# Kernel tuning notes

Measured on AMD Instinct MI355X. Metric: run time of the kernel, lower is better.

The kernel has to match this reference:

```python
import jax, jax.numpy as jnp
import numpy as np

D_THRE = 0.1       # compatibility distance threshold
RATIO = 1.0        # fraction of points kept as seeds
NUM_ITERS = 10     # power-iteration steps
NMS_RADIUS = 0.1   # NMS suppression radius
N_PTS = 6144


def _pairwise_dist(p):
    # p: [N, d] -> [N, N] euclidean distance matrix
    diff = p[:, None, :] - p[None, :, :]
    return jnp.linalg.norm(diff, axis=-1)


def setup_inputs() -> dict:
    key = jax.random.key(0)
    k1, k2 = jax.random.split(key)
    ipts2d = jax.random.uniform(k1, (N_PTS, 2), dtype=jnp.float32)
    ipts3d = jax.random.uniform(k2, (N_PTS, 3), dtype=jnp.float32)
    return {"ipts2d": ipts2d, "ipts3d": ipts3d}


def reference(ipts2d, ipts3d):
    N = ipts2d.shape[0]
    p2d_dist = _pairwise_dist(ipts2d)[None]            # [1, N, N]
    p3d_dist = _pairwise_dist(ipts3d)[None]            # [1, N, N]
    cross_dist = jnp.abs(p2d_dist - p3d_dist)          # [1, N, N]
    SC_measure = jnp.clip(1.0 - cross_dist ** 2 / D_THRE ** 2, 0.0, None)
    hard_SC = (cross_dist < D_THRE).astype(jnp.float32)

    # leading eigenvector via power iteration (fixed iteration count;
    # the torch allclose early-exit is a perf shortcut, same math)
    v0 = jnp.ones((1, N, 1), dtype=SC_measure.dtype)

    def body(i, v):
        v = jnp.matmul(SC_measure, v)                  # [1, N, 1]
        return v / (jnp.linalg.norm(v, axis=1, keepdims=True) + 1e-6)

    v = jax.lax.fori_loop(0, NUM_ITERS, body, v0)
    confidence = v[..., 0]                             # [1, N]

    # NMS seed picking (bs = 1)
    scores = confidence
    score_relation = (scores.T >= scores) | (p2d_dist[0] >= NMS_RADIUS)
    is_local_max = jnp.min(score_relation, axis=-1).astype(jnp.float32)
    score_local_max = scores * is_local_max            # [1, N]
    max_num = int(N * RATIO)
    seeds = jnp.argsort(-score_local_max, axis=1)[:, :max_num]  # [1, max_num]

    # seed gather + dense GEMM (computed as in the original; output unused)
    hard_SC_tight = (cross_dist < D_THRE / 2).astype(jnp.float32)
    seed_hard = hard_SC[:, seeds[0], :]                # [1, max_num, N]
    seed_hard_tight = hard_SC_tight[:, seeds[0], :]    # [1, max_num, N]
    SC2_measure = jnp.matmul(seed_hard_tight, hard_SC_tight) * seed_hard
    del SC2_measure  # original discards it and returns confidence

    return confidence
```

## Files before the change

### kernel.cpp

```cpp
#include <hip/hip_runtime.h>

#define NPTS 6144
#define RESCALE (1.0f / 1024.0f)

#define NIB 24
#define NJB 24
#define BI  256
#define BJ  256
#define MI  4
#define JT  (BJ / 16)
#define ROWU 20
#define LDS_U32 (2 * BJ * ROWU + BJ)

typedef unsigned short u16;
typedef unsigned int   u32;
typedef float v2f    __attribute__((ext_vector_type(2)));
typedef short bf16x8 __attribute__((ext_vector_type(8)));
typedef float f32x4  __attribute__((ext_vector_type(4)));

__device__ __forceinline__ u16 bsplit(float& x) {
  u32 u = __float_as_uint(x) & 0xFFFF0000u;
  x -= __uint_as_float(u);
  return (u16)(u >> 16);
}
__device__ __forceinline__ u32 pk(u16 lo, u16 hi) { return (u32)lo | ((u32)hi << 16); }

__device__ __forceinline__ void build_i(float x2, float y2, float x3, float y3,
                                        float z3, u32* __restrict__ a2,
                                        u32* __restrict__ a3) {
  float n2 = fmaf(x2, x2, y2 * y2);
  float n3 = fmaf(x3, x3, fmaf(y3, y3, z3 * z3));
  const u16 ONE = 0x3F80;
  float t;
  t = -2.f * x2; u16 AXH = bsplit(t), AXM = bsplit(t), AXL = bsplit(t);
  t = -2.f * y2; u16 AYH = bsplit(t), AYM = bsplit(t), AYL = bsplit(t);
  t = n2;        u16 N2H = bsplit(t), N2M = bsplit(t), N2L = bsplit(t);
  t = -2.f * x3; u16 CXH = bsplit(t), CXM = bsplit(t), CXL = bsplit(t);
  t = -2.f * y3; u16 CYH = bsplit(t), CYM = bsplit(t), CYL = bsplit(t);
  t = -2.f * z3; u16 CZH = bsplit(t), CZM = bsplit(t), CZL = bsplit(t);
  t = n3;        u16 N3H = bsplit(t), N3M = bsplit(t), N3L = bsplit(t);
  a2[0] = pk(AXH, AYH); a2[1] = pk(AXM, AYM); a2[2] = pk(AXH, AYH); a2[3] = pk(AXM, AYM);
  a2[4] = pk(AXL, AYL); a2[5] = pk(AXH, AYH); a2[6] = pk(N2H, N2M); a2[7] = pk(N2L, ONE);
  a2[8] = pk(ONE, ONE);
#pragma unroll
  for (int q = 9; q < 16; ++q) a2[q] = 0u;
  a3[0] = pk(CXH, CYH); a3[1]  = pk(CZH, CXM); a3[2]  = pk(CYM, CZM); a3[3]  = pk(CXH, CYH);
  a3[4] = pk(CZH, CXM); a3[5]  = pk(CYM, CZM); a3[6]  = pk(CXL, CYL); a3[7]  = pk(CZL, CXH);
  a3[8] = pk(CYH, CZH); a3[9]  = pk(N3H, N3M); a3[10] = pk(N3L, ONE); a3[11] = pk(ONE, ONE);
#pragma unroll
  for (int q = 12; q < 16; ++q) a3[q] = 0u;
}

__device__ __forceinline__ void build_j(float x2, float y2, float x3, float y3,
                                        float z3, u32* __restrict__ b2,
                                        u32* __restrict__ b3) {
  float n2 = fmaf(x2, x2, y2 * y2);
  float n3 = fmaf(x3, x3, fmaf(y3, y3, z3 * z3));
  const u16 ONE = 0x3F80;
  float t;
  t = x2; u16 BXH = bsplit(t), BXM = bsplit(t), BXL = bsplit(t);
  t = y2; u16 BYH = bsplit(t), BYM = bsplit(t), BYL = bsplit(t);
  t = n2; u16 N2H = bsplit(t), N2M = bsplit(t), N2L = bsplit(t);
  t = x3; u16 DXH = bsplit(t), DXM = bsplit(t), DXL = bsplit(t);
  t = y3; u16 DYH = bsplit(t), DYM = bsplit(t), DYL = bsplit(t);
  t = z3; u16 DZH = bsplit(t), DZM = bsplit(t), DZL = bsplit(t);
  t = n3; u16 N3H = bsplit(t), N3M = bsplit(t), N3L = bsplit(t);
  b2[0] = pk(BXH, BYH); b2[1] = pk(BXH, BYH); b2[2] = pk(BXM, BYM); b2[3] = pk(BXM, BYM);
  b2[4] = pk(BXH, BYH); b2[5] = pk(BXL, BYL); b2[6] = pk(ONE, ONE); b2[7] = pk(ONE, N2H);
  b2[8] = pk(N2M, N2L);
#pragma unroll
  for (int q = 9; q < 16; ++q) b2[q] = 0u;
  b3[0] = pk(DXH, DYH); b3[1]  = pk(DZH, DXH); b3[2]  = pk(DYH, DZH); b3[3]  = pk(DXM, DYM);
  b3[4] = pk(DZM, DXM); b3[5]  = pk(DYM, DZM); b3[6]  = pk(DXH, DYH); b3[7]  = pk(DZH, DXL);
  b3[8] = pk(DYL, DZL); b3[9]  = pk(ONE, ONE); b3[10] = pk(ONE, N3H); b3[11] = pk(N3M, N3L);
#pragma unroll
  for (int q = 12; q < 16; ++q) b3[q] = 0u;
}

__global__ __launch_bounds__(256) void prep_kernel(float* __restrict__ vA,
                                                   float* __restrict__ vB) {
  int i = blockIdx.x * 256 + threadIdx.x;
  vA[i] = 1.0f;
  vB[i] = 0.0f;
}

__global__ __launch_bounds__(256, 2) void matvec_kernel(
    const float* __restrict__ p2, const float* __restrict__ p3,
    const float* __restrict__ vsrc, float* __restrict__ vdst,
    float* __restrict__ vzero) {
  __shared__ u32 sh[LDS_U32];
  float* shf = (float*)sh;
  const int ib = blockIdx.x % NIB;
  const int jb = blockIdx.x / NIB;
  const int t    = threadIdx.x;
  const int lane = t & 63;
  const int wv   = t >> 6;
  const int col  = lane & 15;
  const int kb   = lane >> 4;

  const int ipt = ib * BI + t;
  const int jpt = jb * BJ + t;
  float ix2 = p2[2 * ipt], iy2 = p2[2 * ipt + 1];
  float ix3 = p3[3 * ipt], iy3 = p3[3 * ipt + 1], iz3 = p3[3 * ipt + 2];
  float jx2 = p2[2 * jpt], jy2 = p2[2 * jpt + 1];
  float jx3 = p3[3 * jpt], jy3 = p3[3 * jpt + 1], jz3 = p3[3 * jpt + 2];
  float vj  = vsrc[jpt];
  if (jb == 0) vzero[ipt] = 0.0f;

  build_i(ix2, iy2, ix3, iy3, iz3, &sh[t * ROWU], &sh[BI * ROWU + t * ROWU]);
  __syncthreads();
  bf16x8 a2f[MI], a3f[MI];
#pragma unroll
  for (int mi = 0; mi < MI; ++mi) {
    const int r = wv * 64 + mi * 16 + col;
    a2f[mi] = *(const bf16x8*)&sh[r * ROWU + kb * 4];
    a3f[mi] = *(const bf16x8*)&sh[BI * ROWU + r * ROWU + kb * 4];
  }
  __syncthreads();
  build_j(jx2, jy2, jx3, jy3, jz3, &sh[t * ROWU], &sh[BJ * ROWU + t * ROWU]);
  shf[2 * BJ * ROWU + t] = vj;
  __syncthreads();

  v2f racc[MI][2];
#pragma unroll
  for (int mi = 0; mi < MI; ++mi) {
    racc[mi][0] = (v2f){0.f, 0.f};
    racc[mi][1] = (v2f){0.f, 0.f};
  }
  const v2f kM100 = (v2f){-100.0f, -100.0f};
  const v2f k200  = (v2f){ 200.0f,  200.0f};
  const v2f kOne  = (v2f){   1.0f,    1.0f};
  const v2f kZero = (v2f){   0.0f,    0.0f};
  const f32x4 z4  = (f32x4){0.f, 0.f, 0.f, 0.f};

  for (int tj = 0; tj < JT; ++tj) {
    const int jrow = tj * 16 + col;
    const bf16x8 b2f = *(const bf16x8*)&sh[jrow * ROWU + kb * 4];
    const bf16x8 b3f = *(const bf16x8*)&sh[BJ * ROWU + jrow * ROWU + kb * 4];
    const float vjs = shf[2 * BJ * ROWU + jrow];
    const v2f vj2 = (v2f){vjs, vjs};
#pragma unroll
    for (int mi = 0; mi < MI; ++mi) {
      f32x4 aacc = __builtin_amdgcn_mfma_f32_16x16x32_bf16(a2f[mi], b2f, z4, 0, 0, 0);
      f32x4 bacc = __builtin_amdgcn_mfma_f32_16x16x32_bf16(a3f[mi], b3f, z4, 0, 0, 0);
#pragma unroll
      for (int p = 0; p < 2; ++p) {
        v2f a = (v2f){aacc[2 * p], aacc[2 * p + 1]};
        v2f b = (v2f){bacc[2 * p], bacc[2 * p + 1]};
        v2f ab = __builtin_elementwise_max(a * b, kZero);
        v2f s  = (v2f){__builtin_amdgcn_sqrtf(ab.x), __builtin_amdgcn_sqrtf(ab.y)};
        v2f w  = __builtin_elementwise_fma(a + b, kM100, kOne);
        w = __builtin_elementwise_fma(s, k200, w);
        w = __builtin_elementwise_max(w, kZero);
        racc[mi][p] = __builtin_elementwise_fma(w, vj2, racc[mi][p]);
      }
    }
  }

#pragma unroll
  for (int mi = 0; mi < MI; ++mi) {
#pragma unroll
    for (int p = 0; p < 2; ++p) {
      float r0 = racc[mi][p].x, r1 = racc[mi][p].y;
      r0 += __shfl_xor(r0, 1); r0 += __shfl_xor(r0, 2);
      r0 += __shfl_xor(r0, 4); r0 += __shfl_xor(r0, 8);
      r1 += __shfl_xor(r1, 1); r1 += __shfl_xor(r1, 2);
      r1 += __shfl_xor(r1, 4); r1 += __shfl_xor(r1, 8);
      if (col == 0) {
        const int row = ib * BI + wv * 64 + mi * 16 + kb * 4 + 2 * p;
        atomicAdd(&vdst[row],     r0 * RESCALE);
        atomicAdd(&vdst[row + 1], r1 * RESCALE);
      }
    }
  }
}

__global__ __launch_bounds__(256) void finalize_kernel(
    const float* __restrict__ v, float* __restrict__ out) {
  const int tid = threadIdx.x;
  float ss = 0.0f;
  for (int k = tid; k < NPTS; k += 256) {
    float x = v[k];
    ss = fmaf(x, x, ss);
  }
  for (int off = 32; off > 0; off >>= 1) ss += __shfl_down(ss, off, 64);
  __shared__ float wsum[4];
  if ((tid & 63) == 0) wsum[tid >> 6] = ss;
  __syncthreads();
  float tot = wsum[0] + wsum[1] + wsum[2] + wsum[3];
  float inv = 1.0f / (sqrtf(tot) + 1e-6f);
  int i = blockIdx.x * 256 + tid;
  out[i] = v[i] * inv;
}

extern "C" void kernel_launch(void* const* d_in, const int* in_sizes, int n_in,
                              void* d_out, int out_size, void* d_ws, size_t ws_size,
                              hipStream_t stream) {
  const float* p2 = (const float*)d_in[0];
  const float* p3 = (const float*)d_in[1];
  float* out = (float*)d_out;

  float* w = (float*)d_ws;
  float* buf[3] = { w, w + 8192, w + 16384 };

  prep_kernel<<<NPTS / 256, 256, 0, stream>>>(buf[0], buf[1]);

  for (int k = 0; k < 10; ++k) {
    matvec_kernel<<<NIB * NJB, 256, 0, stream>>>(
        p2, p3, buf[k % 3], buf[(k + 1) % 3], buf[(k + 2) % 3]);
  }

  finalize_kernel<<<NPTS / 256, 256, 0, stream>>>(buf[1], out);
}
```

Before: 238.0 us.

## Exploit symmetry of the compatibility matrix with triangular block tiling

The matvec kernel now processes only the upper-triangular block pairs of the symmetric SC matrix, using 128x128 tiles and a triangular block-index decode. Each off-diagonal tile computes its weights once and accumulates both the row product (w·vj) and the transposed column product (w·vi). The column product is reduced across lanes and added atomically per j-tile. This roughly halves the MFMA and elementwise work per iteration, at the cost of more atomics, an extra shuffle reduction per tile, smaller tiles and a higher occupancy target.

```diff
diff --git a/kernel.cpp b/kernel.cpp
--- a/kernel.cpp
+++ b/kernel.cpp
@@ -3,14 +3,17 @@
 #define NPTS 6144
 #define RESCALE (1.0f / 1024.0f)
 
-#define NIB 24
-#define NJB 24
-#define BI  256
-#define BJ  256
-#define MI  4
-#define JT  (BJ / 16)
+#define NB   48
+#define BT   128
+#define NBLK (NB * (NB + 1) / 2)
+#define MI   2
+#define JT   8
 #define ROWU 20
-#define LDS_U32 (2 * BJ * ROWU + BJ)
+#define OFF_A  0
+#define OFF_B  (2 * BT * ROWU)
+#define OFF_VJ (4 * BT * ROWU)
+#define OFF_VI (4 * BT * ROWU + BT)
+#define LDS_U32 (4 * BT * ROWU + 2 * BT)
 
 typedef unsigned short u16;
 typedef unsigned int   u32;
@@ -84,42 +87,59 @@
   vB[i] = 0.0f;
 }
 
-__global__ __launch_bounds__(256, 2) void matvec_kernel(
+__global__ __launch_bounds__(256, 3) void matvec_kernel(
     const float* __restrict__ p2, const float* __restrict__ p3,
     const float* __restrict__ vsrc, float* __restrict__ vdst,
     float* __restrict__ vzero) {
   __shared__ u32 sh[LDS_U32];
   float* shf = (float*)sh;
-  const int ib = blockIdx.x % NIB;
-  const int jb = blockIdx.x / NIB;
+
+  int k = blockIdx.x;
+  int r = (int)((sqrtf(8.f * (float)k + 1.f) - 1.f) * 0.5f);
+  while ((r + 1) * (r + 2) / 2 <= k) ++r;
+  while (r * (r + 1) / 2 > k) --r;
+  const int ib = k - r * (r + 1) / 2;
+  const int jb = r;
+  const bool offd = (ib != jb);
+
   const int t    = threadIdx.x;
   const int lane = t & 63;
   const int wv   = t >> 6;
   const int col  = lane & 15;
   const int kb   = lane >> 4;
 
-  const int ipt = ib * BI + t;
-  const int jpt = jb * BJ + t;
-  float ix2 = p2[2 * ipt], iy2 = p2[2 * ipt + 1];
-  float ix3 = p3[3 * ipt], iy3 = p3[3 * ipt + 1], iz3 = p3[3 * ipt + 2];
-  float jx2 = p2[2 * jpt], jy2 = p2[2 * jpt + 1];
-  float jx3 = p3[3 * jpt], jy3 = p3[3 * jpt + 1], jz3 = p3[3 * jpt + 2];
-  float vj  = vsrc[jpt];
-  if (jb == 0) vzero[ipt] = 0.0f;
-
-  build_i(ix2, iy2, ix3, iy3, iz3, &sh[t * ROWU], &sh[BI * ROWU + t * ROWU]);
+  if (t < BT) {
+    const int ip = ib * BT + t;
+    float x2 = p2[2 * ip], y2 = p2[2 * ip + 1];
+    float x3 = p3[3 * ip], y3 = p3[3 * ip + 1], z3 = p3[3 * ip + 2];
+    build_i(x2, y2, x3, y3, z3, &sh[OFF_A + t * ROWU],
+            &sh[OFF_A + BT * ROWU + t * ROWU]);
+    shf[OFF_VI + t] = vsrc[ip];
+  } else {
+    const int tt = t - BT;
+    const int jp = jb * BT + tt;
+    float x2 = p2[2 * jp], y2 = p2[2 * jp + 1];
+    float x3 = p3[3 * jp], y3 = p3[3 * jp + 1], z3 = p3[3 * jp + 2];
+    build_j(x2, y2, x3, y3, z3, &sh[OFF_B + tt * ROWU],
+            &sh[OFF_B + BT * ROWU + tt * ROWU]);
+    shf[OFF_VJ + tt] = vsrc[jp];
+  }
+  if (blockIdx.x < 24) vzero[blockIdx.x * 256 + t] = 0.0f;
   __syncthreads();
+
   bf16x8 a2f[MI], a3f[MI];
+  v2f vi2[MI][2];
 #pragma unroll
   for (int mi = 0; mi < MI; ++mi) {
-    const int r = wv * 64 + mi * 16 + col;
-    a2f[mi] = *(const bf16x8*)&sh[r * ROWU + kb * 4];
-    a3f[mi] = *(const bf16x8*)&sh[BI * ROWU + r * ROWU + kb * 4];
-  }
-  __syncthreads();
-  build_j(jx2, jy2, jx3, jy3, jz3, &sh[t * ROWU], &sh[BJ * ROWU + t * ROWU]);
-  shf[2 * BJ * ROWU + t] = vj;
-  __syncthreads();
+    const int rr = wv * 32 + mi * 16 + col;
+    a2f[mi] = *(const bf16x8*)&sh[OFF_A + rr * ROWU + kb * 4];
+    a3f[mi] = *(const bf16x8*)&sh[OFF_A + BT * ROWU + rr * ROWU + kb * 4];
+#pragma unroll
+    for (int p = 0; p < 2; ++p) {
+      const int re = wv * 32 + mi * 16 + kb * 4 + 2 * p;
+      vi2[mi][p] = (v2f){shf[OFF_VI + re], shf[OFF_VI + re + 1]};
+    }
+  }
 
   v2f racc[MI][2];
 #pragma unroll
@@ -133,12 +153,14 @@
   const v2f kZero = (v2f){   0.0f,    0.0f};
   const f32x4 z4  = (f32x4){0.f, 0.f, 0.f, 0.f};
 
+#pragma unroll
   for (int tj = 0; tj < JT; ++tj) {
     const int jrow = tj * 16 + col;
-    const bf16x8 b2f = *(const bf16x8*)&sh[jrow * ROWU + kb * 4];
-    const bf16x8 b3f = *(const bf16x8*)&sh[BJ * ROWU + jrow * ROWU + kb * 4];
-    const float vjs = shf[2 * BJ * ROWU + jrow];
+    const bf16x8 b2f = *(const bf16x8*)&sh[OFF_B + jrow * ROWU + kb * 4];
+    const bf16x8 b3f = *(const bf16x8*)&sh[OFF_B + BT * ROWU + jrow * ROWU + kb * 4];
+    const float vjs = shf[OFF_VJ + jrow];
     const v2f vj2 = (v2f){vjs, vjs};
+    v2f cacc = (v2f){0.f, 0.f};
 #pragma unroll
     for (int mi = 0; mi < MI; ++mi) {
       f32x4 aacc = __builtin_amdgcn_mfma_f32_16x16x32_bf16(a2f[mi], b2f, z4, 0, 0, 0);
@@ -153,7 +175,14 @@
         w = __builtin_elementwise_fma(s, k200, w);
         w = __builtin_elementwise_max(w, kZero);
         racc[mi][p] = __builtin_elementwise_fma(w, vj2, racc[mi][p]);
+        if (offd) cacc = __builtin_elementwise_fma(w, vi2[mi][p], cacc);
       }
+    }
+    if (offd) {
+      float c = cacc.x + cacc.y;
+      c += __shfl_xor(c, 16);
+      c += __shfl_xor(c, 32);
+      if (lane < 16) atomicAdd(&vdst[jb * BT + tj * 16 + lane], c * RESCALE);
     }
   }
 
@@ -167,7 +196,7 @@
       r1 += __shfl_xor(r1, 1); r1 += __shfl_xor(r1, 2);
       r1 += __shfl_xor(r1, 4); r1 += __shfl_xor(r1, 8);
       if (col == 0) {
-        const int row = ib * BI + wv * 64 + mi * 16 + kb * 4 + 2 * p;
+        const int row = ib * BT + wv * 32 + mi * 16 + kb * 4 + 2 * p;
         atomicAdd(&vdst[row],     r0 * RESCALE);
         atomicAdd(&vdst[row + 1], r1 * RESCALE);
       }
@@ -206,7 +235,7 @@
   prep_kernel<<<NPTS / 256, 256, 0, stream>>>(buf[0], buf[1]);
 
   for (int k = 0; k < 10; ++k) {
-    matvec_kernel<<<NIB * NJB, 256, 0, stream>>>(
+    matvec_kernel<<<NBLK, 256, 0, stream>>>(
         p2, p3, buf[k % 3], buf[(k + 1) % 3], buf[(k + 2) % 3]);
   }
 
```

After: 227.5 us. 4.4% less time.
